# Kernel tuning notes

Hardware: AMD Instinct MI355X
Metric: run time of the kernel (lower is better)

The kernel has to match this reference:

```python
import jax, jax.numpy as jnp
import numpy as np

VAR_EPS = 1e-05


def setup_inputs() -> dict:
    key = jax.random.key(0)
    k1, k2 = jax.random.split(key)
    B, T = 1024, 16384
    pred = jax.random.normal(k1, (B, T), dtype=jnp.float32)
    target = jax.random.normal(k2, (B, T), dtype=jnp.float32)
    return {"pred": pred, "target": target}


def reference(pred, target):
    # Per-row Pearson correlation, vectorized over the batch dimension.
    T = pred.shape[1]
    mp = jnp.mean(pred, axis=1, keepdims=True)
    mt = jnp.mean(target, axis=1, keepdims=True)
    cp = pred - mp                      # [B, T] centered
    ct = target - mt
    sp = jnp.sum(cp * cp, axis=1)       # [B] sum of squares
    st = jnp.sum(ct * ct, axis=1)
    num = jnp.sum(cp * ct, axis=1)      # [B] covariance numerator
    # torch.var uses unbiased estimator (correction=1)
    var_p = sp / (T - 1)
    var_t = st / (T - 1)
    denom = jnp.sqrt(sp * st)
    safe_denom = jnp.where(denom > 0, denom, 1.0)
    corr = num / safe_denom
    valid = (var_p > VAR_EPS) & (var_t > VAR_EPS) & (denom > 0) & ~jnp.isnan(corr)
    per_row = jnp.where(valid, 1.0 - corr, 1.0)
    return jnp.mean(per_row)
```

## Files before the change

### kernel.cpp

```cpp
#include <hip/hip_runtime.h>

#define T_LEN 16384
#define Q4    1024
#define VAR_EPS 1e-5f

__global__ __launch_bounds__(256) void pearson_partial_kernel(
    const float* __restrict__ pred, const float* __restrict__ target,
    float* __restrict__ moments)
{
    const int blk = blockIdx.x;
    const int row = blk >> 2;
    const int q   = blk & 3;
    const int tid = threadIdx.x;

    const float4* __restrict__ p4 =
        (const float4*)(pred + (size_t)row * T_LEN) + q * Q4;
    const float4* __restrict__ t4 =
        (const float4*)(target + (size_t)row * T_LEN) + q * Q4;

    float4 a0 = p4[tid];
    float4 a1 = p4[tid + 256];
    float4 a2 = p4[tid + 512];
    float4 a3 = p4[tid + 768];
    float4 b0 = t4[tid];
    float4 b1 = t4[tid + 256];
    float4 b2 = t4[tid + 512];
    float4 b3 = t4[tid + 768];

    float sp  = (a0.x + a0.y + a0.z + a0.w) + (a1.x + a1.y + a1.z + a1.w)
              + (a2.x + a2.y + a2.z + a2.w) + (a3.x + a3.y + a3.z + a3.w);
    float st  = (b0.x + b0.y + b0.z + b0.w) + (b1.x + b1.y + b1.z + b1.w)
              + (b2.x + b2.y + b2.z + b2.w) + (b3.x + b3.y + b3.z + b3.w);
    float spp = a0.x*a0.x + a0.y*a0.y + a0.z*a0.z + a0.w*a0.w
              + a1.x*a1.x + a1.y*a1.y + a1.z*a1.z + a1.w*a1.w
              + a2.x*a2.x + a2.y*a2.y + a2.z*a2.z + a2.w*a2.w
              + a3.x*a3.x + a3.y*a3.y + a3.z*a3.z + a3.w*a3.w;
    float stt = b0.x*b0.x + b0.y*b0.y + b0.z*b0.z + b0.w*b0.w
              + b1.x*b1.x + b1.y*b1.y + b1.z*b1.z + b1.w*b1.w
              + b2.x*b2.x + b2.y*b2.y + b2.z*b2.z + b2.w*b2.w
              + b3.x*b3.x + b3.y*b3.y + b3.z*b3.z + b3.w*b3.w;
    float spt = a0.x*b0.x + a0.y*b0.y + a0.z*b0.z + a0.w*b0.w
              + a1.x*b1.x + a1.y*b1.y + a1.z*b1.z + a1.w*b1.w
              + a2.x*b2.x + a2.y*b2.y + a2.z*b2.z + a2.w*b2.w
              + a3.x*b3.x + a3.y*b3.y + a3.z*b3.z + a3.w*b3.w;

    #pragma unroll
    for (int off = 32; off > 0; off >>= 1) {
        sp  += __shfl_down(sp,  off);
        st  += __shfl_down(st,  off);
        spp += __shfl_down(spp, off);
        stt += __shfl_down(stt, off);
        spt += __shfl_down(spt, off);
    }

    if ((tid & 63) == 0) {
        float* m = moments + row * 8;
        atomicAdd(m + 0, sp);
        atomicAdd(m + 1, st);
        atomicAdd(m + 2, spp);
        atomicAdd(m + 3, stt);
        atomicAdd(m + 4, spt);
    }
}

__global__ __launch_bounds__(1024) void pearson_final_kernel(
    const float* __restrict__ moments, float* __restrict__ out, int B)
{
    const int tid = threadIdx.x;
    float loss_sum = 0.f;

    for (int r = tid; r < B; r += 1024) {
        const float* m = moments + r * 8;
        float S_p  = m[0];
        float S_t  = m[1];
        float S_pp = m[2];
        float S_tt = m[3];
        float S_pt = m[4];

        const float T   = (float)T_LEN;
        const float inv = 1.0f / T;
        float cp2 = S_pp - S_p * S_p * inv;
        float ct2 = S_tt - S_t * S_t * inv;
        float num = S_pt - S_p * S_t * inv;

        float var_p = cp2 / (T - 1.0f);
        float var_t = ct2 / (T - 1.0f);
        float denom = sqrtf(cp2 * ct2);
        float safe  = (denom > 0.0f) ? denom : 1.0f;
        float corr  = num / safe;
        bool valid = (var_p > VAR_EPS) && (var_t > VAR_EPS) &&
                     (denom > 0.0f) && !isnan(corr);
        loss_sum += valid ? (1.0f - corr) : 1.0f;
    }

    #pragma unroll
    for (int off = 32; off > 0; off >>= 1)
        loss_sum += __shfl_down(loss_sum, off);

    __shared__ float ws[16];
    if ((tid & 63) == 0) ws[tid >> 6] = loss_sum;
    __syncthreads();

    if (tid == 0) {
        float tot = 0.f;
        #pragma unroll
        for (int w = 0; w < 16; ++w) tot += ws[w];
        out[0] = tot / (float)B;
    }
}

extern "C" void kernel_launch(void* const* d_in, const int* in_sizes, int n_in,
                              void* d_out, int out_size, void* d_ws, size_t ws_size,
                              hipStream_t stream) {
    const float* pred   = (const float*)d_in[0];
    const float* target = (const float*)d_in[1];
    float* out     = (float*)d_out;
    float* moments = (float*)d_ws;

    const int B = in_sizes[0] / T_LEN;

    hipMemsetAsync(moments, 0, (size_t)B * 8 * sizeof(float), stream);
    pearson_partial_kernel<<<B * 4, 256, 0, stream>>>(pred, target, moments);
    pearson_final_kernel<<<1, 1024, 0, stream>>>(moments, out, B);
}
```

Before: 144.3 us.

## Use one block per row with double-buffered loads, dropping memset and atomics

Each block now handles a whole row (four chunks) and double-buffers float4 loads so the next chunk's loads are in flight while the current one accumulates. Per-row moments are reduced in shared memory and the per-row loss is computed in the same kernel. This removes the hipMemsetAsync launch and the global atomicAdds. The cost is four times fewer blocks (1024) and higher register pressure from holding 16 float4 values per thread, which may lower occupancy and memory-level parallelism.

```diff
diff --git a/kernel.cpp b/kernel.cpp
--- a/kernel.cpp
+++ b/kernel.cpp
@@ -1,48 +1,60 @@
 #include <hip/hip_runtime.h>
 
 #define T_LEN 16384
-#define Q4    1024
 #define VAR_EPS 1e-5f
 
-__global__ __launch_bounds__(256) void pearson_partial_kernel(
+
+#define LOAD8(P0,P1,P2,P3,Q0,Q1,Q2,Q3,BASE)        \
+    P0 = p4[(BASE) + tid];                          \
+    P1 = p4[(BASE) + tid + 256];                    \
+    P2 = p4[(BASE) + tid + 512];                    \
+    P3 = p4[(BASE) + tid + 768];                    \
+    Q0 = t4[(BASE) + tid];                          \
+    Q1 = t4[(BASE) + tid + 256];                    \
+    Q2 = t4[(BASE) + tid + 512];                    \
+    Q3 = t4[(BASE) + tid + 768];
+
+#define ACC8(P0,P1,P2,P3,Q0,Q1,Q2,Q3)                                        \
+    sp  += (P0.x + P0.y + P0.z + P0.w) + (P1.x + P1.y + P1.z + P1.w)         \
+         + (P2.x + P2.y + P2.z + P2.w) + (P3.x + P3.y + P3.z + P3.w);        \
+    st  += (Q0.x + Q0.y + Q0.z + Q0.w) + (Q1.x + Q1.y + Q1.z + Q1.w)         \
+         + (Q2.x + Q2.y + Q2.z + Q2.w) + (Q3.x + Q3.y + Q3.z + Q3.w);        \
+    spp += P0.x*P0.x + P0.y*P0.y + P0.z*P0.z + P0.w*P0.w                     \
+         + P1.x*P1.x + P1.y*P1.y + P1.z*P1.z + P1.w*P1.w                     \
+         + P2.x*P2.x + P2.y*P2.y + P2.z*P2.z + P2.w*P2.w                     \
+         + P3.x*P3.x + P3.y*P3.y + P3.z*P3.z + P3.w*P3.w;                    \
+    stt += Q0.x*Q0.x + Q0.y*Q0.y + Q0.z*Q0.z + Q0.w*Q0.w                     \
+         + Q1.x*Q1.x + Q1.y*Q1.y + Q1.z*Q1.z + Q1.w*Q1.w                     \
+         + Q2.x*Q2.x + Q2.y*Q2.y + Q2.z*Q2.z + Q2.w*Q2.w                     \
+         + Q3.x*Q3.x + Q3.y*Q3.y + Q3.z*Q3.z + Q3.w*Q3.w;                    \
+    spt += P0.x*Q0.x + P0.y*Q0.y + P0.z*Q0.z + P0.w*Q0.w                     \
+         + P1.x*Q1.x + P1.y*Q1.y + P1.z*Q1.z + P1.w*Q1.w                     \
+         + P2.x*Q2.x + P2.y*Q2.y + P2.z*Q2.z + P2.w*Q2.w                     \
+         + P3.x*Q3.x + P3.y*Q3.y + P3.z*Q3.z + P3.w*Q3.w;
+
+__global__ __launch_bounds__(256) void pearson_row_kernel(
     const float* __restrict__ pred, const float* __restrict__ target,
-    float* __restrict__ moments)
+    float* __restrict__ loss)
 {
-    const int blk = blockIdx.x;
-    const int row = blk >> 2;
-    const int q   = blk & 3;
+    const int row = blockIdx.x;
     const int tid = threadIdx.x;
 
-    const float4* __restrict__ p4 =
-        (const float4*)(pred + (size_t)row * T_LEN) + q * Q4;
-    const float4* __restrict__ t4 =
-        (const float4*)(target + (size_t)row * T_LEN) + q * Q4;
+    const float4* __restrict__ p4 = (const float4*)(pred   + (size_t)row * T_LEN);
+    const float4* __restrict__ t4 = (const float4*)(target + (size_t)row * T_LEN);
 
-    float4 a0 = p4[tid];
-    float4 a1 = p4[tid + 256];
-    float4 a2 = p4[tid + 512];
-    float4 a3 = p4[tid + 768];
-    float4 b0 = t4[tid];
-    float4 b1 = t4[tid + 256];
-    float4 b2 = t4[tid + 512];
-    float4 b3 = t4[tid + 768];
+    float sp = 0.f, st = 0.f, spp = 0.f, stt = 0.f, spt = 0.f;
 
-    float sp  = (a0.x + a0.y + a0.z + a0.w) + (a1.x + a1.y + a1.z + a1.w)
-              + (a2.x + a2.y + a2.z + a2.w) + (a3.x + a3.y + a3.z + a3.w);
-    float st  = (b0.x + b0.y + b0.z + b0.w) + (b1.x + b1.y + b1.z + b1.w)
-              + (b2.x + b2.y + b2.z + b2.w) + (b3.x + b3.y + b3.z + b3.w);
-    float spp = a0.x*a0.x + a0.y*a0.y + a0.z*a0.z + a0.w*a0.w
-              + a1.x*a1.x + a1.y*a1.y + a1.z*a1.z + a1.w*a1.w
-              + a2.x*a2.x + a2.y*a2.y + a2.z*a2.z + a2.w*a2.w
-              + a3.x*a3.x + a3.y*a3.y + a3.z*a3.z + a3.w*a3.w;
-    float stt = b0.x*b0.x + b0.y*b0.y + b0.z*b0.z + b0.w*b0.w
-              + b1.x*b1.x + b1.y*b1.y + b1.z*b1.z + b1.w*b1.w
-              + b2.x*b2.x + b2.y*b2.y + b2.z*b2.z + b2.w*b2.w
-              + b3.x*b3.x + b3.y*b3.y + b3.z*b3.z + b3.w*b3.w;
-    float spt = a0.x*b0.x + a0.y*b0.y + a0.z*b0.z + a0.w*b0.w
-              + a1.x*b1.x + a1.y*b1.y + a1.z*b1.z + a1.w*b1.w
-              + a2.x*b2.x + a2.y*b2.y + a2.z*b2.z + a2.w*b2.w
-              + a3.x*b3.x + a3.y*b3.y + a3.z*b3.z + a3.w*b3.w;
+    float4 pa0, pa1, pa2, pa3, ta0, ta1, ta2, ta3;
+    float4 pb0, pb1, pb2, pb3, tb0, tb1, tb2, tb3;
+
+    LOAD8(pa0, pa1, pa2, pa3, ta0, ta1, ta2, ta3, 0)
+    LOAD8(pb0, pb1, pb2, pb3, tb0, tb1, tb2, tb3, 1024)
+    ACC8 (pa0, pa1, pa2, pa3, ta0, ta1, ta2, ta3)
+    LOAD8(pa0, pa1, pa2, pa3, ta0, ta1, ta2, ta3, 2048)
+    ACC8 (pb0, pb1, pb2, pb3, tb0, tb1, tb2, tb3)
+    LOAD8(pb0, pb1, pb2, pb3, tb0, tb1, tb2, tb3, 3072)
+    ACC8 (pa0, pa1, pa2, pa3, ta0, ta1, ta2, ta3)
+    ACC8 (pb0, pb1, pb2, pb3, tb0, tb1, tb2, tb3)
 
     #pragma unroll
     for (int off = 32; off > 0; off >>= 1) {
@@ -53,29 +65,20 @@
         spt += __shfl_down(spt, off);
     }
 
+    __shared__ float ws[4][8];
+    const int wid = tid >> 6;
     if ((tid & 63) == 0) {
-        float* m = moments + row * 8;
-        atomicAdd(m + 0, sp);
-        atomicAdd(m + 1, st);
-        atomicAdd(m + 2, spp);
-        atomicAdd(m + 3, stt);
-        atomicAdd(m + 4, spt);
+        ws[wid][0] = sp;  ws[wid][1] = st;  ws[wid][2] = spp;
+        ws[wid][3] = stt; ws[wid][4] = spt;
     }
-}
+    __syncthreads();
 
-__global__ __launch_bounds__(1024) void pearson_final_kernel(
-    const float* __restrict__ moments, float* __restrict__ out, int B)
-{
-    const int tid = threadIdx.x;
-    float loss_sum = 0.f;
-
-    for (int r = tid; r < B; r += 1024) {
-        const float* m = moments + r * 8;
-        float S_p  = m[0];
-        float S_t  = m[1];
-        float S_pp = m[2];
-        float S_tt = m[3];
-        float S_pt = m[4];
+    if (tid == 0) {
+        float S_p  = ws[0][0] + ws[1][0] + ws[2][0] + ws[3][0];
+        float S_t  = ws[0][1] + ws[1][1] + ws[2][1] + ws[3][1];
+        float S_pp = ws[0][2] + ws[1][2] + ws[2][2] + ws[3][2];
+        float S_tt = ws[0][3] + ws[1][3] + ws[2][3] + ws[3][3];
+        float S_pt = ws[0][4] + ws[1][4] + ws[2][4] + ws[3][4];
 
         const float T   = (float)T_LEN;
         const float inv = 1.0f / T;
@@ -90,23 +93,27 @@
         float corr  = num / safe;
         bool valid = (var_p > VAR_EPS) && (var_t > VAR_EPS) &&
                      (denom > 0.0f) && !isnan(corr);
-        loss_sum += valid ? (1.0f - corr) : 1.0f;
+        loss[row] = valid ? (1.0f - corr) : 1.0f;
     }
+}
+
+__global__ __launch_bounds__(256) void pearson_mean_kernel(
+    const float* __restrict__ loss, float* __restrict__ out, int B)
+{
+    const int tid = threadIdx.x;
+    float s = 0.f;
+    for (int r = tid; r < B; r += 256) s += loss[r];
 
     #pragma unroll
     for (int off = 32; off > 0; off >>= 1)
-        loss_sum += __shfl_down(loss_sum, off);
+        s += __shfl_down(s, off);
 
-    __shared__ float ws[16];
-    if ((tid & 63) == 0) ws[tid >> 6] = loss_sum;
+    __shared__ float ws[4];
+    if ((tid & 63) == 0) ws[tid >> 6] = s;
     __syncthreads();
 
-    if (tid == 0) {
-        float tot = 0.f;
-        #pragma unroll
-        for (int w = 0; w < 16; ++w) tot += ws[w];
-        out[0] = tot / (float)B;
-    }
+    if (tid == 0)
+        out[0] = (ws[0] + ws[1] + ws[2] + ws[3]) / (float)B;
 }
 
 extern "C" void kernel_launch(void* const* d_in, const int* in_sizes, int n_in,
@@ -114,12 +121,11 @@
                               hipStream_t stream) {
     const float* pred   = (const float*)d_in[0];
     const float* target = (const float*)d_in[1];
-    float* out     = (float*)d_out;
-    float* moments = (float*)d_ws;
+    float* out  = (float*)d_out;
+    float* lossbuf = (float*)d_ws;
 
     const int B = in_sizes[0] / T_LEN;
 
-    hipMemsetAsync(moments, 0, (size_t)B * 8 * sizeof(float), stream);
-    pearson_partial_kernel<<<B * 4, 256, 0, stream>>>(pred, target, moments);
-    pearson_final_kernel<<<1, 1024, 0, stream>>>(moments, out, B);
+    pearson_row_kernel<<<B, 256, 0, stream>>>(pred, target, lossbuf);
+    pearson_mean_kernel<<<1, 256, 0, stream>>>(lossbuf, out, B);
 }
```

Measured after the change: 146.0 us. About the same (+1.2%).

## Use half-row blocks with nontemporal loads and drop atomics and memset

Applied to the files above, without the earlier changes.

Each block now covers half a row (8 float4 pairs per thread, loaded with a software-prefetch pattern) rather than a quarter, which halves the grid. Loads go through nontemporal builtins so the streamed data avoids polluting the cache. Per-block partial moments are combined in shared memory and written directly to per-block slots, so the global atomics and the hipMemsetAsync launch are no longer needed. The final kernel sums the two halves itself. The trade-off is fewer blocks and higher register pressure per thread in exchange for lower launch and atomic overhead.

```diff
diff --git a/kernel.cpp b/kernel.cpp
--- a/kernel.cpp
+++ b/kernel.cpp
@@ -1,48 +1,48 @@
 #include <hip/hip_runtime.h>
 
 #define T_LEN 16384
-#define Q4    1024
 #define VAR_EPS 1e-5f
 
-__global__ __launch_bounds__(256) void pearson_partial_kernel(
+typedef float v4 __attribute__((ext_vector_type(4)));
+#define NTL(P) __builtin_nontemporal_load(P)
+
+
+#define ACC(P,Q)                                              \
+    sp  += (P.x + P.y) + (P.z + P.w);                         \
+    st  += (Q.x + Q.y) + (Q.z + Q.w);                         \
+    spp += P.x*P.x + P.y*P.y + P.z*P.z + P.w*P.w;             \
+    stt += Q.x*Q.x + Q.y*Q.y + Q.z*Q.z + Q.w*Q.w;             \
+    spt += P.x*Q.x + P.y*Q.y + P.z*Q.z + P.w*Q.w;
+
+__global__ __launch_bounds__(256) void pearson_half_kernel(
     const float* __restrict__ pred, const float* __restrict__ target,
     float* __restrict__ moments)
 {
-    const int blk = blockIdx.x;
-    const int row = blk >> 2;
-    const int q   = blk & 3;
-    const int tid = threadIdx.x;
+    const int blk  = blockIdx.x;
+    const int row  = blk >> 1;
+    const int half = blk & 1;
+    const int tid  = threadIdx.x;
 
-    const float4* __restrict__ p4 =
-        (const float4*)(pred + (size_t)row * T_LEN) + q * Q4;
-    const float4* __restrict__ t4 =
-        (const float4*)(target + (size_t)row * T_LEN) + q * Q4;
+    const v4* __restrict__ p4 =
+        (const v4*)(pred   + (size_t)row * T_LEN) + half * 2048;
+    const v4* __restrict__ t4 =
+        (const v4*)(target + (size_t)row * T_LEN) + half * 2048;
 
-    float4 a0 = p4[tid];
-    float4 a1 = p4[tid + 256];
-    float4 a2 = p4[tid + 512];
-    float4 a3 = p4[tid + 768];
-    float4 b0 = t4[tid];
-    float4 b1 = t4[tid + 256];
-    float4 b2 = t4[tid + 512];
-    float4 b3 = t4[tid + 768];
+    float sp = 0.f, st = 0.f, spp = 0.f, stt = 0.f, spt = 0.f;
 
-    float sp  = (a0.x + a0.y + a0.z + a0.w) + (a1.x + a1.y + a1.z + a1.w)
-              + (a2.x + a2.y + a2.z + a2.w) + (a3.x + a3.y + a3.z + a3.w);
-    float st  = (b0.x + b0.y + b0.z + b0.w) + (b1.x + b1.y + b1.z + b1.w)
-              + (b2.x + b2.y + b2.z + b2.w) + (b3.x + b3.y + b3.z + b3.w);
-    float spp = a0.x*a0.x + a0.y*a0.y + a0.z*a0.z + a0.w*a0.w
-              + a1.x*a1.x + a1.y*a1.y + a1.z*a1.z + a1.w*a1.w
-              + a2.x*a2.x + a2.y*a2.y + a2.z*a2.z + a2.w*a2.w
-              + a3.x*a3.x + a3.y*a3.y + a3.z*a3.z + a3.w*a3.w;
-    float stt = b0.x*b0.x + b0.y*b0.y + b0.z*b0.z + b0.w*b0.w
-              + b1.x*b1.x + b1.y*b1.y + b1.z*b1.z + b1.w*b1.w
-              + b2.x*b2.x + b2.y*b2.y + b2.z*b2.z + b2.w*b2.w
-              + b3.x*b3.x + b3.y*b3.y + b3.z*b3.z + b3.w*b3.w;
-    float spt = a0.x*b0.x + a0.y*b0.y + a0.z*b0.z + a0.w*b0.w
-              + a1.x*b1.x + a1.y*b1.y + a1.z*b1.z + a1.w*b1.w
-              + a2.x*b2.x + a2.y*b2.y + a2.z*b2.z + a2.w*b2.w
-              + a3.x*b3.x + a3.y*b3.y + a3.z*b3.z + a3.w*b3.w;
+    v4 p0 = NTL(p4 + tid);        v4 t0 = NTL(t4 + tid);
+    v4 p1 = NTL(p4 + tid + 256);  v4 t1 = NTL(t4 + tid + 256);
+    v4 p2 = NTL(p4 + tid + 512);  v4 t2 = NTL(t4 + tid + 512);
+    v4 p3 = NTL(p4 + tid + 768);  v4 t3 = NTL(t4 + tid + 768);
+
+    ACC(p0, t0); p0 = NTL(p4 + tid + 1024); t0 = NTL(t4 + tid + 1024);
+    ACC(p1, t1); p1 = NTL(p4 + tid + 1280); t1 = NTL(t4 + tid + 1280);
+    ACC(p2, t2); p2 = NTL(p4 + tid + 1536); t2 = NTL(t4 + tid + 1536);
+    ACC(p3, t3); p3 = NTL(p4 + tid + 1792); t3 = NTL(t4 + tid + 1792);
+    ACC(p0, t0);
+    ACC(p1, t1);
+    ACC(p2, t2);
+    ACC(p3, t3);
 
     #pragma unroll
     for (int off = 32; off > 0; off >>= 1) {
@@ -53,13 +53,21 @@
         spt += __shfl_down(spt, off);
     }
 
+    __shared__ float ws[4][8];
+    const int wid = tid >> 6;
     if ((tid & 63) == 0) {
-        float* m = moments + row * 8;
-        atomicAdd(m + 0, sp);
-        atomicAdd(m + 1, st);
-        atomicAdd(m + 2, spp);
-        atomicAdd(m + 3, stt);
-        atomicAdd(m + 4, spt);
+        ws[wid][0] = sp;  ws[wid][1] = st;  ws[wid][2] = spp;
+        ws[wid][3] = stt; ws[wid][4] = spt;
+    }
+    __syncthreads();
+
+    if (tid == 0) {
+        float* m = moments + (size_t)blk * 8;
+        m[0] = ws[0][0] + ws[1][0] + ws[2][0] + ws[3][0];
+        m[1] = ws[0][1] + ws[1][1] + ws[2][1] + ws[3][1];
+        m[2] = ws[0][2] + ws[1][2] + ws[2][2] + ws[3][2];
+        m[3] = ws[0][3] + ws[1][3] + ws[2][3] + ws[3][3];
+        m[4] = ws[0][4] + ws[1][4] + ws[2][4] + ws[3][4];
     }
 }
 
@@ -70,12 +78,13 @@
     float loss_sum = 0.f;
 
     for (int r = tid; r < B; r += 1024) {
-        const float* m = moments + r * 8;
-        float S_p  = m[0];
-        float S_t  = m[1];
-        float S_pp = m[2];
-        float S_tt = m[3];
-        float S_pt = m[4];
+        const float* m0 = moments + (size_t)r * 16;
+        const float* m1 = m0 + 8;
+        float S_p  = m0[0] + m1[0];
+        float S_t  = m0[1] + m1[1];
+        float S_pp = m0[2] + m1[2];
+        float S_tt = m0[3] + m1[3];
+        float S_pt = m0[4] + m1[4];
 
         const float T   = (float)T_LEN;
         const float inv = 1.0f / T;
@@ -119,7 +128,6 @@
 
     const int B = in_sizes[0] / T_LEN;
 
-    hipMemsetAsync(moments, 0, (size_t)B * 8 * sizeof(float), stream);
-    pearson_partial_kernel<<<B * 4, 256, 0, stream>>>(pred, target, moments);
+    pearson_half_kernel<<<B * 2, 256, 0, stream>>>(pred, target, moments);
     pearson_final_kernel<<<1, 1024, 0, stream>>>(moments, out, B);
 }
```

After: 138.7 us. -3.9%, faster.
